# Optimization experiments

Hardware: AMD Instinct MI355X
Metric: run time of the kernel (lower is better)

## Reference

```python
import jax, jax.numpy as jnp
import numpy as np

N_COARSE = 200000
N_FINE = 800000
E = 3200000
EP = 2400000
C_IN = 128
C_OUT = 64


def setup_inputs() -> dict:
    key = jax.random.key(0)
    ks = jax.random.split(key, 8)
    x = jax.random.normal(ks[0], (N_COARSE, C_IN), dtype=jnp.float32)
    edge_index = jax.random.randint(ks[1], (2, E), 0, N_COARSE, dtype=jnp.int64)
    edge_attr = jax.random.uniform(ks[2], (E, 1), dtype=jnp.float32)
    pool_src = jax.random.randint(ks[3], (EP,), 0, N_COARSE, dtype=jnp.int64)
    pool_dst = jax.random.randint(ks[4], (EP,), 0, N_FINE, dtype=jnp.int64)
    pool_edge_attr = jax.random.uniform(ks[5], (EP, 1), dtype=jnp.float32)
    scale = 1.0 / np.sqrt(C_IN)
    W_root = jax.random.normal(ks[6], (C_IN, C_OUT), dtype=jnp.float32) * scale
    W_nbr = jax.random.normal(ks[7], (C_IN, C_OUT), dtype=jnp.float32) * scale
    b = jnp.zeros((C_OUT,), dtype=jnp.float32)
    return {
        "x": x, "W_root": W_root, "W_nbr": W_nbr, "b": b,
        "edge_index": edge_index, "edge_attr": edge_attr,
        "pool_src": pool_src, "pool_dst": pool_dst,
        "pool_edge_attr": pool_edge_attr, "n_fine": N_FINE,
    }


def reference(x, W_root, W_nbr, b, edge_index, edge_attr, pool_src, pool_dst, pool_edge_attr, n_fine):
    # --- CustomGraphConvPointPoint ---
    # self term: [Nc, C_OUT]
    h = x @ W_root + b
    # neighbor messages: transform once, then gather per-edge and weight by edge_attr
    m = x @ W_nbr                      # [Nc, C_OUT]
    src, dst = edge_index[0], edge_index[1]
    msg = m[src] * edge_attr           # [E, C_OUT], edge_attr broadcasts over channels
    agg = jax.ops.segment_sum(msg, dst, num_segments=N_COARSE)  # [Nc, C_OUT]
    h = h + agg
    # --- CustomUnpooling: scatter coarse features to fine nodes, weighted ---
    fine_msg = h[pool_src] * pool_edge_attr                     # [EP, C_OUT]
    y = jax.ops.segment_sum(fine_msg, pool_dst, num_segments=n_fine)  # [Nf, C_OUT]
    return y
```

## Files before the change

### kernel.cpp

```cpp
#include <hip/hip_runtime.h>

#define CIN 128
#define COUT 64

__global__ __launch_bounds__(256) void gemm_hm_kernel(
        const float* __restrict__ x,
        const float* __restrict__ Wr,
        const float* __restrict__ Wn,
        const float* __restrict__ b,
        float* __restrict__ h,
        float* __restrict__ m,
        int n_coarse) {
    __shared__ float xs[32][CIN];
    const int rowBase = blockIdx.x * 32;

    if (rowBase + 32 <= n_coarse) {
        const float4* x4 = (const float4*)(x + (long long)rowBase * CIN);
        float4* xs4 = (float4*)&xs[0][0];
        for (int i = threadIdx.x; i < 32 * (CIN / 4); i += 256) xs4[i] = x4[i];
    } else {
        for (int i = threadIdx.x; i < 32 * CIN; i += 256) {
            int r = i / CIN, k = i % CIN;
            int row = rowBase + r;
            xs[r][k] = (row < n_coarse) ? x[(long long)row * CIN + k] : 0.f;
        }
    }
    __syncthreads();

    const int wv = threadIdx.x >> 6;
    const int c  = threadIdx.x & 63;
    const int r0 = wv * 8;

    float ah[8], am[8];
    const float bias = b[c];
#pragma unroll
    for (int j = 0; j < 8; ++j) { ah[j] = bias; am[j] = 0.f; }

    for (int k = 0; k < CIN; k += 4) {
        const float wr0 = Wr[(k + 0) * COUT + c];
        const float wr1 = Wr[(k + 1) * COUT + c];
        const float wr2 = Wr[(k + 2) * COUT + c];
        const float wr3 = Wr[(k + 3) * COUT + c];
        const float wn0 = Wn[(k + 0) * COUT + c];
        const float wn1 = Wn[(k + 1) * COUT + c];
        const float wn2 = Wn[(k + 2) * COUT + c];
        const float wn3 = Wn[(k + 3) * COUT + c];
#pragma unroll
        for (int j = 0; j < 8; ++j) {
            const float4 xv = *(const float4*)&xs[r0 + j][k];
            ah[j] = fmaf(xv.x, wr0, ah[j]);
            ah[j] = fmaf(xv.y, wr1, ah[j]);
            ah[j] = fmaf(xv.z, wr2, ah[j]);
            ah[j] = fmaf(xv.w, wr3, ah[j]);
            am[j] = fmaf(xv.x, wn0, am[j]);
            am[j] = fmaf(xv.y, wn1, am[j]);
            am[j] = fmaf(xv.z, wn2, am[j]);
            am[j] = fmaf(xv.w, wn3, am[j]);
        }
    }

#pragma unroll
    for (int j = 0; j < 8; ++j) {
        const int row = rowBase + r0 + j;
        if (row < n_coarse) {
            h[row * COUT + c] = ah[j];
            m[row * COUT + c] = am[j];
        }
    }
}

__global__ __launch_bounds__(256) void hist_kernel(
        const int* __restrict__ dst, int* __restrict__ cnt, int n) {
    const int e = blockIdx.x * 256 + threadIdx.x;
    if (e < n) atomicAdd(&cnt[dst[e]], 1);
}

__global__ __launch_bounds__(256) void assign_base_kernel(
        const int* __restrict__ cnt, int* __restrict__ base,
        int* __restrict__ fill, int* __restrict__ cursor, int n) {
    __shared__ int s[256];
    __shared__ int blockBase;
    const int tid = threadIdx.x;
    const int i = blockIdx.x * 256 + tid;
    const int v = (i < n) ? cnt[i] : 0;
    s[tid] = v;
    __syncthreads();
#pragma unroll
    for (int off = 1; off < 256; off <<= 1) {
        int t = (tid >= off) ? s[tid - off] : 0;
        __syncthreads();
        if (tid >= off) s[tid] += t;
        __syncthreads();
    }
    if (tid == 255) blockBase = atomicAdd(cursor, s[255]);
    __syncthreads();
    if (i < n) {
        const int bse = blockBase + s[tid] - v;
        base[i] = bse;
        fill[i] = bse;
    }
}

__global__ __launch_bounds__(256) void scatter_kernel(
        const int* __restrict__ src, const int* __restrict__ dst,
        const float* __restrict__ w, int* __restrict__ fill,
        int2* __restrict__ edges, int n) {
    const int e = blockIdx.x * 256 + threadIdx.x;
    if (e >= n) return;
    const int d = dst[e];
    const int pos = atomicAdd(&fill[d], 1);
    edges[pos] = make_int2(src[e] * COUT, __float_as_int(w[e]));
}

__global__ __launch_bounds__(256) void csr_gather_add_kernel(
        const float* __restrict__ m,
        const int* __restrict__ base, const int* __restrict__ cnt,
        const int2* __restrict__ edges,
        float* __restrict__ h, int n_rows) {
    const int row = blockIdx.x * 4 + (threadIdx.x >> 6);
    const int c = threadIdx.x & 63;
    if (row >= n_rows) return;
    const int p = base[row];
    const int n = cnt[row];
    float acc = 0.f;
    int j = 0;
    for (; j + 4 <= n; j += 4) {
        const int2 e0 = edges[p + j + 0];
        const int2 e1 = edges[p + j + 1];
        const int2 e2 = edges[p + j + 2];
        const int2 e3 = edges[p + j + 3];
        const float v0 = m[e0.x + c];
        const float v1 = m[e1.x + c];
        const float v2 = m[e2.x + c];
        const float v3 = m[e3.x + c];
        acc = fmaf(v0, __int_as_float(e0.y), acc);
        acc = fmaf(v1, __int_as_float(e1.y), acc);
        acc = fmaf(v2, __int_as_float(e2.y), acc);
        acc = fmaf(v3, __int_as_float(e3.y), acc);
    }
    for (; j < n; ++j) {
        const int2 e0 = edges[p + j];
        acc = fmaf(m[e0.x + c], __int_as_float(e0.y), acc);
    }
    h[row * COUT + c] += acc;
}

__global__ __launch_bounds__(256) void csr_gather_write_kernel(
        const float* __restrict__ h,
        const int* __restrict__ base, const int* __restrict__ cnt,
        const int2* __restrict__ edges,
        float* __restrict__ y, int n_rows) {
    const int row = blockIdx.x * 4 + (threadIdx.x >> 6);
    const int c = threadIdx.x & 63;
    if (row >= n_rows) return;
    const int p = base[row];
    const int n = cnt[row];
    float acc = 0.f;
    int j = 0;
    for (; j + 4 <= n; j += 4) {
        const int2 e0 = edges[p + j + 0];
        const int2 e1 = edges[p + j + 1];
        const int2 e2 = edges[p + j + 2];
        const int2 e3 = edges[p + j + 3];
        const float v0 = h[e0.x + c];
        const float v1 = h[e1.x + c];
        const float v2 = h[e2.x + c];
        const float v3 = h[e3.x + c];
        acc = fmaf(v0, __int_as_float(e0.y), acc);
        acc = fmaf(v1, __int_as_float(e1.y), acc);
        acc = fmaf(v2, __int_as_float(e2.y), acc);
        acc = fmaf(v3, __int_as_float(e3.y), acc);
    }
    for (; j < n; ++j) {
        const int2 e0 = edges[p + j];
        acc = fmaf(h[e0.x + c], __int_as_float(e0.y), acc);
    }
    y[row * COUT + c] = acc;
}

extern "C" void kernel_launch(void* const* d_in, const int* in_sizes, int n_in,
                              void* d_out, int out_size, void* d_ws, size_t ws_size,
                              hipStream_t stream) {
    const float* x      = (const float*)d_in[0];
    const float* W_root = (const float*)d_in[1];
    const float* W_nbr  = (const float*)d_in[2];
    const float* b      = (const float*)d_in[3];
    const int*   eidx   = (const int*)d_in[4];
    const float* eattr  = (const float*)d_in[5];
    const int*   psrc   = (const int*)d_in[6];
    const int*   pdst   = (const int*)d_in[7];
    const float* pattr  = (const float*)d_in[8];

    const int n_coarse = in_sizes[0] / CIN;
    const int n_edges  = in_sizes[4] / 2;
    const int n_pool   = in_sizes[6];
    const int n_fine   = out_size / COUT;

    const int* esrc = eidx;
    const int* edst = eidx + n_edges;

    float* h = (float*)d_ws;
    float* m = h + (size_t)n_coarse * COUT;

    char* outb = (char*)d_out;
    int2* edges1  = (int2*)outb;
    char* p1      = outb + (size_t)n_edges * sizeof(int2);
    int*  cnt1    = (int*)p1;
    int*  cursor1 = (int*)(p1 + (size_t)n_coarse * 4);
    int*  base1   = (int*)(p1 + (size_t)n_coarse * 4 + 16);
    int*  fill1   = (int*)(p1 + (size_t)n_coarse * 4 + 16 + (size_t)n_coarse * 4);

    char* mb      = (char*)m;
    int2* edges2  = (int2*)mb;
    char* p2      = mb + (size_t)n_pool * sizeof(int2);
    int*  cnt2    = (int*)p2;
    int*  cursor2 = (int*)(p2 + (size_t)n_fine * 4);
    int*  base2   = (int*)(p2 + (size_t)n_fine * 4 + 16);
    int*  fill2   = (int*)(p2 + (size_t)n_fine * 4 + 16 + (size_t)n_fine * 4);

    gemm_hm_kernel<<<(n_coarse + 31) / 32, 256, 0, stream>>>(x, W_root, W_nbr, b, h, m, n_coarse);

    hipMemsetAsync(cnt1, 0, (size_t)n_coarse * 4 + 16, stream);
    hist_kernel<<<(n_edges + 255) / 256, 256, 0, stream>>>(edst, cnt1, n_edges);
    assign_base_kernel<<<(n_coarse + 255) / 256, 256, 0, stream>>>(cnt1, base1, fill1, cursor1, n_coarse);
    scatter_kernel<<<(n_edges + 255) / 256, 256, 0, stream>>>(esrc, edst, eattr, fill1, edges1, n_edges);

    csr_gather_add_kernel<<<(n_coarse + 3) / 4, 256, 0, stream>>>(
        m, base1, cnt1, edges1, h, n_coarse);

    hipMemsetAsync(cnt2, 0, (size_t)n_fine * 4 + 16, stream);
    hist_kernel<<<(n_pool + 255) / 256, 256, 0, stream>>>(pdst, cnt2, n_pool);
    assign_base_kernel<<<(n_fine + 255) / 256, 256, 0, stream>>>(cnt2, base2, fill2, cursor2, n_fine);
    scatter_kernel<<<(n_pool + 255) / 256, 256, 0, stream>>>(psrc, pdst, pattr, fill2, edges2, n_pool);

    csr_gather_write_kernel<<<(n_fine + 3) / 4, 256, 0, stream>>>(
        h, base2, cnt2, edges2, (float*)d_out, n_fine);
}
```

Baseline: 1.370 ms.

## Partition histogram and scatter atomics by destination range per XCD

The histogram and scatter kernels become grid-stride kernels in which each block, picked by blockIdx modulo 8, handles only destinations in one eighth of the node range. Because blocks are dispatched round-robin across the 8 XCDs, atomics to a given counter range stay within one XCD's L2, which is meant to avoid cross-die coherence traffic on the atomics. The cost is that every block re-reads the whole dst array (8x the index reads) and src/w are read with scattered scalar loads. The speedup depends on the round-robin block-to-XCD mapping, which the hardware does not guarantee.

```diff
diff --git a/kernel.cpp b/kernel.cpp
--- a/kernel.cpp
+++ b/kernel.cpp
@@ -2,6 +2,7 @@
 
 #define CIN 128
 #define COUT 64
+#define NXCD 8
 
 __global__ __launch_bounds__(256) void gemm_hm_kernel(
         const float* __restrict__ x,
@@ -69,10 +70,29 @@
     }
 }
 
-__global__ __launch_bounds__(256) void hist_kernel(
-        const int* __restrict__ dst, int* __restrict__ cnt, int n) {
-    const int e = blockIdx.x * 256 + threadIdx.x;
-    if (e < n) atomicAdd(&cnt[dst[e]], 1);
+__global__ __launch_bounds__(256) void hist_xcd_kernel(
+        const int* __restrict__ dst, int* __restrict__ cnt, int n, int rpr) {
+    const int range = blockIdx.x & (NXCD - 1);
+    const int lo = range * rpr;
+    const int hi = lo + rpr;
+    const int tpr = (gridDim.x >> 3) * 256;
+    const int ng = (n + 3) >> 2;
+    const int4* __restrict__ dst4 = (const int4*)dst;
+    for (int g = (blockIdx.x >> 3) * 256 + threadIdx.x; g < ng; g += tpr) {
+        const int e0 = g << 2;
+        if (e0 + 3 < n) {
+            const int4 d4 = dst4[g];
+            if (d4.x >= lo && d4.x < hi) atomicAdd(&cnt[d4.x], 1);
+            if (d4.y >= lo && d4.y < hi) atomicAdd(&cnt[d4.y], 1);
+            if (d4.z >= lo && d4.z < hi) atomicAdd(&cnt[d4.z], 1);
+            if (d4.w >= lo && d4.w < hi) atomicAdd(&cnt[d4.w], 1);
+        } else {
+            for (int k = 0; k < 4 && e0 + k < n; ++k) {
+                const int d = dst[e0 + k];
+                if (d >= lo && d < hi) atomicAdd(&cnt[d], 1);
+            }
+        }
+    }
 }
 
 __global__ __launch_bounds__(256) void assign_base_kernel(
@@ -101,15 +121,41 @@
     }
 }
 
-__global__ __launch_bounds__(256) void scatter_kernel(
+__global__ __launch_bounds__(256) void scatter_xcd_kernel(
         const int* __restrict__ src, const int* __restrict__ dst,
         const float* __restrict__ w, int* __restrict__ fill,
-        int2* __restrict__ edges, int n) {
-    const int e = blockIdx.x * 256 + threadIdx.x;
-    if (e >= n) return;
-    const int d = dst[e];
-    const int pos = atomicAdd(&fill[d], 1);
-    edges[pos] = make_int2(src[e] * COUT, __float_as_int(w[e]));
+        int2* __restrict__ edges, int n, int rpr) {
+    const int range = blockIdx.x & (NXCD - 1);
+    const int lo = range * rpr;
+    const int hi = lo + rpr;
+    const int tpr = (gridDim.x >> 3) * 256;
+    const int ng = (n + 3) >> 2;
+    const int4* __restrict__ dst4 = (const int4*)dst;
+    for (int g = (blockIdx.x >> 3) * 256 + threadIdx.x; g < ng; g += tpr) {
+        const int e0 = g << 2;
+        if (e0 + 3 < n) {
+            const int4 d4 = dst4[g];
+            const int dd[4] = {d4.x, d4.y, d4.z, d4.w};
+#pragma unroll
+            for (int k = 0; k < 4; ++k) {
+                const int d = dd[k];
+                if (d >= lo && d < hi) {
+                    const int pos = atomicAdd(&fill[d], 1);
+                    edges[pos] = make_int2(src[e0 + k] * COUT,
+                                           __float_as_int(w[e0 + k]));
+                }
+            }
+        } else {
+            for (int k = 0; k < 4 && e0 + k < n; ++k) {
+                const int d = dst[e0 + k];
+                if (d >= lo && d < hi) {
+                    const int pos = atomicAdd(&fill[d], 1);
+                    edges[pos] = make_int2(src[e0 + k] * COUT,
+                                           __float_as_int(w[e0 + k]));
+                }
+            }
+        }
+    }
 }
 
 __global__ __launch_bounds__(256) void csr_gather_add_kernel(
@@ -218,20 +264,23 @@
     int*  base2   = (int*)(p2 + (size_t)n_fine * 4 + 16);
     int*  fill2   = (int*)(p2 + (size_t)n_fine * 4 + 16 + (size_t)n_fine * 4);
 
+    const int rpr1 = (n_coarse + NXCD - 1) / NXCD;
+    const int rpr2 = (n_fine + NXCD - 1) / NXCD;
+
     gemm_hm_kernel<<<(n_coarse + 31) / 32, 256, 0, stream>>>(x, W_root, W_nbr, b, h, m, n_coarse);
 
     hipMemsetAsync(cnt1, 0, (size_t)n_coarse * 4 + 16, stream);
-    hist_kernel<<<(n_edges + 255) / 256, 256, 0, stream>>>(edst, cnt1, n_edges);
+    hist_xcd_kernel<<<2048, 256, 0, stream>>>(edst, cnt1, n_edges, rpr1);
     assign_base_kernel<<<(n_coarse + 255) / 256, 256, 0, stream>>>(cnt1, base1, fill1, cursor1, n_coarse);
-    scatter_kernel<<<(n_edges + 255) / 256, 256, 0, stream>>>(esrc, edst, eattr, fill1, edges1, n_edges);
+    scatter_xcd_kernel<<<2048, 256, 0, stream>>>(esrc, edst, eattr, fill1, edges1, n_edges, rpr1);
 
     csr_gather_add_kernel<<<(n_coarse + 3) / 4, 256, 0, stream>>>(
         m, base1, cnt1, edges1, h, n_coarse);
 
     hipMemsetAsync(cnt2, 0, (size_t)n_fine * 4 + 16, stream);
-    hist_kernel<<<(n_pool + 255) / 256, 256, 0, stream>>>(pdst, cnt2, n_pool);
+    hist_xcd_kernel<<<2048, 256, 0, stream>>>(pdst, cnt2, n_pool, rpr2);
     assign_base_kernel<<<(n_fine + 255) / 256, 256, 0, stream>>>(cnt2, base2, fill2, cursor2, n_fine);
-    scatter_kernel<<<(n_pool + 255) / 256, 256, 0, stream>>>(psrc, pdst, pattr, fill2, edges2, n_pool);
+    scatter_xcd_kernel<<<2048, 256, 0, stream>>>(psrc, pdst, pattr, fill2, edges2, n_pool, rpr2);
 
     csr_gather_write_kernel<<<(n_fine + 3) / 4, 256, 0, stream>>>(
         h, base2, cnt2, edges2, (float*)d_out, n_fine);
```

Result: faster. 1.297 ms (-5.3%).
